# Kernel tuning notes

Measured on AMD Instinct MI355X. Metric: run time of the kernel, lower is better.

Reference implementation:

```python
import jax, jax.numpy as jnp
import numpy as np


def _safe_div(w, n):
    # tf.math.divide_no_nan: returns 0 where denominator is 0
    n = n[:, None]
    return jnp.where(n > 0, w / jnp.where(n > 0, n, 1.0), 0.0)


def setup_inputs() -> dict:
    key = jax.random.key(0)
    x = jax.random.normal(key, (16, 32768, 256), dtype=jnp.float32)
    return {"x": x}


def reference(x):
    # x: [n_models, n_samples, dim]
    n_models = x.shape[0]
    xt = jnp.transpose(x, (1, 0, 2))  # [ns, nm, dim]
    v0 = xt[:, 0, :]
    basis_list = [_safe_div(v0, jnp.linalg.norm(v0, axis=1))]  # each [ns, dim]
    for i in range(1, n_models):
        B = jnp.stack(basis_list, axis=1)              # [ns, i, dim]
        v = xt[:, i, :]                                # [ns, dim]
        coef = jnp.einsum('nd,nid->ni', v, B)          # projections onto basis
        w = v - jnp.einsum('ni,nid->nd', coef, B)      # classical Gram-Schmidt step
        basis_list.append(_safe_div(w, jnp.linalg.norm(w, axis=1)))
    return jnp.stack(basis_list, axis=0)               # [n_models, ns, dim]
```

## Files before the change

kernel.cpp:

```cpp
#include <hip/hip_runtime.h>
#include <hip/hip_bf16.h>


constexpr int NM   = 16;
constexpr int NR   = 32768;
constexpr int D4   = 64;
constexpr int FROW = 132;

typedef __attribute__((ext_vector_type(8))) short short8v;
typedef __attribute__((ext_vector_type(4))) float f32x4;

__device__ __forceinline__ float rl(float x, int lane) {
    return __builtin_bit_cast(float,
        __builtin_amdgcn_readlane(__builtin_bit_cast(int, x), lane));
}

__device__ __forceinline__ void cvt8(const float4& f0, const float4& f1,
                                     short8v& ah, short8v& al) {
    float f[8] = {f0.x, f0.y, f0.z, f0.w, f1.x, f1.y, f1.z, f1.w};
#pragma unroll
    for (int j = 0; j < 8; ++j) {
        unsigned short hb =
            __builtin_bit_cast(unsigned short, __float2bfloat16(f[j]));
        ah[j] = (short)hb;
        float hv = __builtin_bit_cast(float, (unsigned int)hb << 16);
        al[j] = (short)__builtin_bit_cast(unsigned short,
                                          __float2bfloat16(f[j] - hv));
    }
}

__global__ __launch_bounds__(64, 4) void gs_kernel(const float* __restrict__ x,
                                                   float* __restrict__ out) {
    __shared__ __align__(16) float sm[NM * FROW];

    const int lane = threadIdx.x;
    const int row  = blockIdx.x;
    const int vec  = lane & 15;
    const int kgrp = lane >> 4;

    const float4* __restrict__ xi = reinterpret_cast<const float4*>(x);
    float4* __restrict__ oo       = reinterpret_cast<float4*>(out);

    float4 v[NM];
#pragma unroll
    for (int i = 0; i < NM; ++i)
        v[i] = xi[(size_t)(i * NR + row) * D4 + lane];

    f32x4 g = {0.0f, 0.0f, 0.0f, 0.0f};
#pragma unroll
    for (int p = 0; p < 2; ++p) {
        if (p) __syncthreads();
        if ((lane >> 5) == p) {
            const int sl = lane & 31;
#pragma unroll
            for (int i = 0; i < NM; ++i)
                *reinterpret_cast<float4*>(&sm[i * FROW + 4 * sl]) = v[i];
        }
        __syncthreads();
#pragma unroll
        for (int c4 = 0; c4 < 4; ++c4) {
            const int off = vec * FROW + c4 * 32 + kgrp * 8;
            float4 f0 = *reinterpret_cast<const float4*>(&sm[off]);
            float4 f1 = *reinterpret_cast<const float4*>(&sm[off + 4]);
            short8v ah, al;
            cvt8(f0, f1, ah, al);
            g = __builtin_amdgcn_mfma_f32_16x16x32_bf16(ah, ah, g, 0, 0, 0);
            g = __builtin_amdgcn_mfma_f32_16x16x32_bf16(ah, al, g, 0, 0, 0);
            g = __builtin_amdgcn_mfma_f32_16x16x32_bf16(al, ah, g, 0, 0, 0);
        }
    }

    float a[NM];
#pragma unroll
    for (int n = 0; n < NM; ++n)
        a[n] = __shfl(g[n & 3], vec + 16 * (n >> 2), 64);

#pragma unroll
    for (int j = 0; j < NM; ++j) {
        float p   = rl(a[j], j);
        float inv = (p > 0.0f) ? rsqrtf(p) : 0.0f;
        v[j].x *= inv; v[j].y *= inv; v[j].z *= inv; v[j].w *= inv;
        oo[(size_t)(j * NR + row) * D4 + lane] = v[j];
        a[j] *= inv;
#pragma unroll
        for (int t = j + 1; t < NM; ++t) {
            float u = rl(a[j], t);
            a[t]  = fmaf(-u, a[j], a[t]);
            v[t].x = fmaf(-u, v[j].x, v[t].x);
            v[t].y = fmaf(-u, v[j].y, v[t].y);
            v[t].z = fmaf(-u, v[j].z, v[t].z);
            v[t].w = fmaf(-u, v[j].w, v[t].w);
        }
    }
}

extern "C" void kernel_launch(void* const* d_in, const int* in_sizes, int n_in,
                              void* d_out, int out_size, void* d_ws, size_t ws_size,
                              hipStream_t stream) {
    const float* x = (const float*)d_in[0];
    float* out     = (float*)d_out;
    dim3 grid(NR);
    dim3 block(64);
    hipLaunchKernelGGL(gs_kernel, grid, block, 0, stream, x, out);
}
```

Measured before the change: 222.3 us.

## Process two rows per wavefront with bf16 split staged once in LDS

```diff
diff --git a/kernel.cpp b/kernel.cpp
--- a/kernel.cpp
+++ b/kernel.cpp
@@ -5,7 +5,7 @@
 constexpr int NM   = 16;
 constexpr int NR   = 32768;
 constexpr int D4   = 64;
-constexpr int FROW = 132;
+constexpr int LROW = 264;
 
 typedef __attribute__((ext_vector_type(8))) short short8v;
 typedef __attribute__((ext_vector_type(4))) float f32x4;
@@ -15,83 +15,100 @@
         __builtin_amdgcn_readlane(__builtin_bit_cast(int, x), lane));
 }
 
-__device__ __forceinline__ void cvt8(const float4& f0, const float4& f1,
-                                     short8v& ah, short8v& al) {
-    float f[8] = {f0.x, f0.y, f0.z, f0.w, f1.x, f1.y, f1.z, f1.w};
-#pragma unroll
-    for (int j = 0; j < 8; ++j) {
-        unsigned short hb =
-            __builtin_bit_cast(unsigned short, __float2bfloat16(f[j]));
-        ah[j] = (short)hb;
-        float hv = __builtin_bit_cast(float, (unsigned int)hb << 16);
-        al[j] = (short)__builtin_bit_cast(unsigned short,
-                                          __float2bfloat16(f[j] - hv));
-    }
-}
-
-__global__ __launch_bounds__(64, 4) void gs_kernel(const float* __restrict__ x,
-                                                   float* __restrict__ out) {
-    __shared__ __align__(16) float sm[NM * FROW];
+__global__ __launch_bounds__(64) void gs_kernel(const float* __restrict__ x,
+                                                float* __restrict__ out) {
+    __shared__ __align__(16) unsigned short sm_hi[NM * LROW];
+    __shared__ __align__(16) unsigned short sm_lo[NM * LROW];
 
     const int lane = threadIdx.x;
-    const int row  = blockIdx.x;
     const int vec  = lane & 15;
     const int kgrp = lane >> 4;
+    const int rowA = blockIdx.x * 2;
+    const int rowB = rowA + 1;
 
     const float4* __restrict__ xi = reinterpret_cast<const float4*>(x);
     float4* __restrict__ oo       = reinterpret_cast<float4*>(out);
 
-    float4 v[NM];
+    float4 vA[NM], vB[NM];
 #pragma unroll
     for (int i = 0; i < NM; ++i)
-        v[i] = xi[(size_t)(i * NR + row) * D4 + lane];
+        vA[i] = xi[(size_t)(i * NR + rowA) * D4 + lane];
+#pragma unroll
+    for (int i = 0; i < NM; ++i)
+        vB[i] = xi[(size_t)(i * NR + rowB) * D4 + lane];
 
-    f32x4 g = {0.0f, 0.0f, 0.0f, 0.0f};
+    auto stage = [&](const float4* v) {
 #pragma unroll
-    for (int p = 0; p < 2; ++p) {
-        if (p) __syncthreads();
-        if ((lane >> 5) == p) {
-            const int sl = lane & 31;
+        for (int i = 0; i < NM; ++i) {
+            float f[4] = {v[i].x, v[i].y, v[i].z, v[i].w};
+            ushort4 hp, lp;
+            unsigned short* hh = &hp.x;
+            unsigned short* ll = &lp.x;
 #pragma unroll
-            for (int i = 0; i < NM; ++i)
-                *reinterpret_cast<float4*>(&sm[i * FROW + 4 * sl]) = v[i];
+            for (int j = 0; j < 4; ++j) {
+                unsigned short hb =
+                    __builtin_bit_cast(unsigned short, __float2bfloat16(f[j]));
+                hh[j] = hb;
+                float hv = __builtin_bit_cast(float, (unsigned int)hb << 16);
+                ll[j] = __builtin_bit_cast(unsigned short,
+                                           __float2bfloat16(f[j] - hv));
+            }
+            *reinterpret_cast<ushort4*>(&sm_hi[i * LROW + 4 * lane]) = hp;
+            *reinterpret_cast<ushort4*>(&sm_lo[i * LROW + 4 * lane]) = lp;
         }
-        __syncthreads();
+    };
+
+    auto gram = [&]() {
+        f32x4 g = {0.0f, 0.0f, 0.0f, 0.0f};
 #pragma unroll
-        for (int c4 = 0; c4 < 4; ++c4) {
-            const int off = vec * FROW + c4 * 32 + kgrp * 8;
-            float4 f0 = *reinterpret_cast<const float4*>(&sm[off]);
-            float4 f1 = *reinterpret_cast<const float4*>(&sm[off + 4]);
-            short8v ah, al;
-            cvt8(f0, f1, ah, al);
+        for (int c = 0; c < 8; ++c) {
+            const int off = vec * LROW + c * 32 + kgrp * 8;
+            short8v ah = *reinterpret_cast<const short8v*>(&sm_hi[off]);
+            short8v al = *reinterpret_cast<const short8v*>(&sm_lo[off]);
             g = __builtin_amdgcn_mfma_f32_16x16x32_bf16(ah, ah, g, 0, 0, 0);
             g = __builtin_amdgcn_mfma_f32_16x16x32_bf16(ah, al, g, 0, 0, 0);
             g = __builtin_amdgcn_mfma_f32_16x16x32_bf16(al, ah, g, 0, 0, 0);
         }
-    }
+        return g;
+    };
 
-    float a[NM];
+    auto solve = [&](f32x4 g, float4* v, int row) {
+        float a[NM];
 #pragma unroll
-    for (int n = 0; n < NM; ++n)
-        a[n] = __shfl(g[n & 3], vec + 16 * (n >> 2), 64);
+        for (int n = 0; n < NM; ++n)
+            a[n] = __shfl(g[n & 3], vec + 16 * (n >> 2), 64);
+#pragma unroll
+        for (int j = 0; j < NM; ++j) {
+            float p   = rl(a[j], j);
+            float inv = (p > 0.0f) ? rsqrtf(p) : 0.0f;
+            v[j].x *= inv; v[j].y *= inv; v[j].z *= inv; v[j].w *= inv;
+            oo[(size_t)(j * NR + row) * D4 + lane] = v[j];
+            a[j] *= inv;
+#pragma unroll
+            for (int t = j + 1; t < NM; ++t) {
+                float u = rl(a[j], t);
+                a[t]  = fmaf(-u, a[j], a[t]);
+                v[t].x = fmaf(-u, v[j].x, v[t].x);
+                v[t].y = fmaf(-u, v[j].y, v[t].y);
+                v[t].z = fmaf(-u, v[j].z, v[t].z);
+                v[t].w = fmaf(-u, v[j].w, v[t].w);
+            }
+        }
+    };
 
-#pragma unroll
-    for (int j = 0; j < NM; ++j) {
-        float p   = rl(a[j], j);
-        float inv = (p > 0.0f) ? rsqrtf(p) : 0.0f;
-        v[j].x *= inv; v[j].y *= inv; v[j].z *= inv; v[j].w *= inv;
-        oo[(size_t)(j * NR + row) * D4 + lane] = v[j];
-        a[j] *= inv;
-#pragma unroll
-        for (int t = j + 1; t < NM; ++t) {
-            float u = rl(a[j], t);
-            a[t]  = fmaf(-u, a[j], a[t]);
-            v[t].x = fmaf(-u, v[j].x, v[t].x);
-            v[t].y = fmaf(-u, v[j].y, v[t].y);
-            v[t].z = fmaf(-u, v[j].z, v[t].z);
-            v[t].w = fmaf(-u, v[j].w, v[t].w);
-        }
-    }
+    stage(vA);
+    asm volatile("s_waitcnt lgkmcnt(0)" ::: "memory");
+    __builtin_amdgcn_sched_barrier(0);
+    f32x4 gA = gram();
+    __builtin_amdgcn_sched_barrier(0);
+
+    stage(vB);
+    asm volatile("s_waitcnt lgkmcnt(0)" ::: "memory");
+    __builtin_amdgcn_sched_barrier(0);
+
+    f32x4 gB = gram();
+    solve(gA, vA, rowA);
+    solve(gB, vB, rowB);
 }
 
 extern "C" void kernel_launch(void* const* d_in, const int* in_sizes, int n_in,
@@ -99,7 +116,7 @@
                               hipStream_t stream) {
     const float* x = (const float*)d_in[0];
     float* out     = (float*)d_out;
-    dim3 grid(NR);
+    dim3 grid(NR / 2);
     dim3 block(64);
     hipLaunchKernelGGL(gs_kernel, grid, block, 0, stream, x, out);
 }
```

Measured after the change: 222.9 us. Within noise of the previous version (+0.2%).

## Make Gram-Schmidt kernel persistent with double-buffered async global-to-LDS prefetch

Applied to the files above, without the earlier changes.

```diff
diff --git a/kernel.cpp b/kernel.cpp
--- a/kernel.cpp
+++ b/kernel.cpp
@@ -5,7 +5,9 @@
 constexpr int NM   = 16;
 constexpr int NR   = 32768;
 constexpr int D4   = 64;
-constexpr int FROW = 132;
+constexpr int FROW = 260;
+constexpr int GRID = 1024;
+constexpr int RPB  = NR / GRID;
 
 typedef __attribute__((ext_vector_type(8))) short short8v;
 typedef __attribute__((ext_vector_type(4))) float f32x4;
@@ -29,68 +31,82 @@
     }
 }
 
-__global__ __launch_bounds__(64, 4) void gs_kernel(const float* __restrict__ x,
-                                                   float* __restrict__ out) {
-    __shared__ __align__(16) float sm[NM * FROW];
+__global__ __launch_bounds__(64) void gs_kernel(const float* __restrict__ x,
+                                                float* __restrict__ out) {
+    __shared__ __align__(16) float sm[2][NM * FROW];
 
     const int lane = threadIdx.x;
-    const int row  = blockIdx.x;
+    const int bid  = blockIdx.x;
     const int vec  = lane & 15;
     const int kgrp = lane >> 4;
 
     const float4* __restrict__ xi = reinterpret_cast<const float4*>(x);
     float4* __restrict__ oo       = reinterpret_cast<float4*>(out);
 
-    float4 v[NM];
+    auto prefetch = [&](int b, int row) {
 #pragma unroll
-    for (int i = 0; i < NM; ++i)
-        v[i] = xi[(size_t)(i * NR + row) * D4 + lane];
+        for (int i = 0; i < NM; ++i) {
+            const float4* src = xi + (size_t)(i * NR + row) * D4 + lane;
+            __builtin_amdgcn_global_load_lds(
+                (const __attribute__((address_space(1))) void*)src,
+                (__attribute__((address_space(3))) void*)&sm[b][i * FROW],
+                16, 0, 0);
+        }
+    };
 
-    f32x4 g = {0.0f, 0.0f, 0.0f, 0.0f};
+    int buf = 0;
+    prefetch(0, bid);
+
+    for (int it = 0; it < RPB; ++it) {
+        const int row = it * GRID + bid;
+
+        asm volatile("s_waitcnt vmcnt(0)" ::: "memory");
+        __builtin_amdgcn_sched_barrier(0);
+
+        if (it + 1 < RPB) prefetch(buf ^ 1, row + GRID);
+
+        f32x4 g = {0.0f, 0.0f, 0.0f, 0.0f};
 #pragma unroll
-    for (int p = 0; p < 2; ++p) {
-        if (p) __syncthreads();
-        if ((lane >> 5) == p) {
-            const int sl = lane & 31;
-#pragma unroll
-            for (int i = 0; i < NM; ++i)
-                *reinterpret_cast<float4*>(&sm[i * FROW + 4 * sl]) = v[i];
-        }
-        __syncthreads();
-#pragma unroll
-        for (int c4 = 0; c4 < 4; ++c4) {
-            const int off = vec * FROW + c4 * 32 + kgrp * 8;
-            float4 f0 = *reinterpret_cast<const float4*>(&sm[off]);
-            float4 f1 = *reinterpret_cast<const float4*>(&sm[off + 4]);
+        for (int c = 0; c < 8; ++c) {
+            const int off = vec * FROW + c * 32 + kgrp * 8;
+            float4 f0 = *reinterpret_cast<const float4*>(&sm[buf][off]);
+            float4 f1 = *reinterpret_cast<const float4*>(&sm[buf][off + 4]);
             short8v ah, al;
             cvt8(f0, f1, ah, al);
             g = __builtin_amdgcn_mfma_f32_16x16x32_bf16(ah, ah, g, 0, 0, 0);
             g = __builtin_amdgcn_mfma_f32_16x16x32_bf16(ah, al, g, 0, 0, 0);
             g = __builtin_amdgcn_mfma_f32_16x16x32_bf16(al, ah, g, 0, 0, 0);
         }
-    }
 
-    float a[NM];
+        float4 v[NM];
 #pragma unroll
-    for (int n = 0; n < NM; ++n)
-        a[n] = __shfl(g[n & 3], vec + 16 * (n >> 2), 64);
+        for (int i = 0; i < NM; ++i)
+            v[i] = *reinterpret_cast<const float4*>(&sm[buf][i * FROW + 4 * lane]);
+
+        float a[NM];
+#pragma unroll
+        for (int n = 0; n < NM; ++n)
+            a[n] = __shfl(g[n & 3], vec + 16 * (n >> 2), 64);
 
 #pragma unroll
-    for (int j = 0; j < NM; ++j) {
-        float p   = rl(a[j], j);
-        float inv = (p > 0.0f) ? rsqrtf(p) : 0.0f;
-        v[j].x *= inv; v[j].y *= inv; v[j].z *= inv; v[j].w *= inv;
-        oo[(size_t)(j * NR + row) * D4 + lane] = v[j];
-        a[j] *= inv;
+        for (int j = 0; j < NM; ++j) {
+            float p   = rl(a[j], j);
+            float inv = (p > 0.0f) ? rsqrtf(p) : 0.0f;
+            v[j].x *= inv; v[j].y *= inv; v[j].z *= inv; v[j].w *= inv;
+            oo[(size_t)(j * NR + row) * D4 + lane] = v[j];
+            a[j] *= inv;
 #pragma unroll
-        for (int t = j + 1; t < NM; ++t) {
-            float u = rl(a[j], t);
-            a[t]  = fmaf(-u, a[j], a[t]);
-            v[t].x = fmaf(-u, v[j].x, v[t].x);
-            v[t].y = fmaf(-u, v[j].y, v[t].y);
-            v[t].z = fmaf(-u, v[j].z, v[t].z);
-            v[t].w = fmaf(-u, v[j].w, v[t].w);
+            for (int t = j + 1; t < NM; ++t) {
+                float u = rl(a[j], t);
+                a[t]  = fmaf(-u, a[j], a[t]);
+                v[t].x = fmaf(-u, v[j].x, v[t].x);
+                v[t].y = fmaf(-u, v[j].y, v[t].y);
+                v[t].z = fmaf(-u, v[j].z, v[t].z);
+                v[t].w = fmaf(-u, v[j].w, v[t].w);
+            }
         }
+
+        buf ^= 1;
     }
 }
 
@@ -99,7 +115,7 @@
                               hipStream_t stream) {
     const float* x = (const float*)d_in[0];
     float* out     = (float*)d_out;
-    dim3 grid(NR);
+    dim3 grid(GRID);
     dim3 block(64);
     hipLaunchKernelGGL(gs_kernel, grid, block, 0, stream, x, out);
 }
```

Result: slower. 227.9 us (+2.5%).
